# Performance work log

Hardware: AMD Instinct MI355X
Metric: run time of the kernel (lower is better)

The kernel has to match this reference:

```python
import jax, jax.numpy as jnp
import numpy as np

B, T, D = 4096, 64, 100   # trajectories, observed time points, feature dim (50 feat + 50 mask)
F = D // 2                # feature half
L = 64                    # latent_dim
NU = 64                   # n_gru_units / n_ode_units
K = 128                   # number of unique event times (integer grid 0..K-1)
DEC = 1                   # decoder output dim (volume)


def setup_inputs() -> dict:
    key = jax.random.key(0)
    ks = jax.random.split(key, 20)
    data = jax.random.normal(ks[0], (B, T, D), dtype=jnp.float32)
    # make mask half non-negative so (sum>0) masking is meaningful
    data = data.at[:, :, F:].set(jnp.abs(data[:, :, F:]))
    time_steps = jnp.sort(jax.random.randint(ks[1], (B, T), 0, K), axis=1)
    s = 0.1
    p = {}
    gi = D // 2 + L  # GRU gate input: latent + feature half
    p['Wu1'] = jax.random.normal(ks[2], (gi, NU), jnp.float32) * s
    p['bu1'] = jnp.zeros((NU,), jnp.float32)
    p['Wu2'] = jax.random.normal(ks[3], (NU, L), jnp.float32) * s
    p['bu2'] = jnp.zeros((L,), jnp.float32)
    p['Wr1'] = jax.random.normal(ks[4], (gi, NU), jnp.float32) * s
    p['br1'] = jnp.zeros((NU,), jnp.float32)
    p['Wr2'] = jax.random.normal(ks[5], (NU, L), jnp.float32) * s
    p['br2'] = jnp.zeros((L,), jnp.float32)
    p['Wn1'] = jax.random.normal(ks[6], (gi, NU), jnp.float32) * s
    p['bn1'] = jnp.zeros((NU,), jnp.float32)
    p['Wn2'] = jax.random.normal(ks[7], (NU, L), jnp.float32) * s
    p['bn2'] = jnp.zeros((L,), jnp.float32)
    # ODE func (tanh MLP), Euler-integrated one step per event interval
    p['Wo1'] = jax.random.normal(ks[8], (L, NU), jnp.float32) * s
    p['bo1'] = jnp.zeros((NU,), jnp.float32)
    p['Wo2'] = jax.random.normal(ks[9], (NU, L), jnp.float32) * s
    p['bo2'] = jnp.zeros((L,), jnp.float32)
    # decoder latent -> volume
    p['Wd'] = jax.random.normal(ks[10], (L, DEC), jnp.float32) * s
    p['bd'] = jnp.zeros((DEC,), jnp.float32)
    return {'data': data, 'time_steps': time_steps, **p}


def reference(data, time_steps,
              Wu1, bu1, Wu2, bu2,
              Wr1, br1, Wr2, br2,
              Wn1, bn1, Wn2, bn2,
              Wo1, bo1, Wo2, bo2,
              Wd, bd):
    f32 = data.dtype
    # pad one zero row at end of time axis (torch: cat(data, zeros[:,1]))
    data_pad = jnp.concatenate([data, jnp.zeros((B, 1, D), f32)], axis=1)  # [B, T+1, D]

    # presence[b, k] = 1 if event time k observed for trajectory b
    presence = jnp.zeros((B, K), f32).at[jnp.arange(B)[:, None], time_steps].set(1.0)
    upd_all = presence.T  # [K, B]  (update_mask per step)
    # fetched_count before step k = number of observed events with time < k
    counts = jnp.concatenate([jnp.zeros((B, 1), f32), jnp.cumsum(presence, axis=1)[:, :-1]], axis=1)
    idx_all = jnp.clip(counts.astype(jnp.int32), 0, T).T  # [K, B]
    rows = jnp.arange(B)

    def step(prev_y, inp):
        idx_i, upd_i = inp  # [B] int, [B] float
        upd = upd_i[:, None]
        # ODE solver: linspace gives 2 points per unit interval -> one Euler step, dt=1
        y1 = prev_y + jnp.tanh(prev_y @ Wo1 + bo1) @ Wo2 + bo2  # ode_sol end
        vol = prev_y @ Wd + bd  # decoder(ode_sol[:, :-1]) mean over single point = decoder(y0)
        fx = data_pad[rows, idx_i] * upd  # dynamic gather + mask  [B, D]
        feat, msk = fx[:, :F], fx[:, F:]
        yc = jnp.concatenate([y1, feat], axis=-1)
        u = jax.nn.sigmoid(jnp.tanh(yc @ Wu1 + bu1) @ Wu2 + bu2)
        r = jax.nn.sigmoid(jnp.tanh(yc @ Wr1 + br1) @ Wr2 + br2)
        cc = jnp.concatenate([y1 * r, feat], axis=-1)
        ns = jnp.tanh(cc @ Wn1 + bn1) @ Wn2 + bn2
        ny = (1.0 - u) * ns + u * y1
        m = (jnp.sum(msk, axis=-1, keepdims=True) > 0).astype(f32)
        ny = m * ny + (1.0 - m) * y1
        prev_y = ny * upd + y1 * (1.0 - upd)
        return prev_y, vol

    prev_y0 = jnp.zeros((B, L), f32)
    prev_y, volume_dt = jax.lax.scan(step, prev_y0, (idx_all, upd_all))
    volume_dt = jnp.transpose(volume_dt, (1, 0, 2))  # [B, K, DEC]

    # inverse_indices == time_steps values on the integer event grid
    inv = jnp.clip(time_steps[:, :-1], 0, K - 2)
    selected_state = jnp.take_along_axis(volume_dt[:, 1:], inv[:, :, None], axis=1)  # [B, T-1, DEC]
    time_intervals = (time_steps[:, 1:] - time_steps[:, :-1]).astype(f32)
    return prev_y, selected_state, time_intervals
```

## Files before the change

### kernel.cpp

```cpp
#include <hip/hip_runtime.h>


typedef __attribute__((ext_vector_type(8))) _Float16 half8;
typedef __attribute__((ext_vector_type(4))) float floatx4;

#define MFMA(a, b, c) __builtin_amdgcn_mfma_f32_16x16x32_f16((a), (b), (c), 0, 0, 0)

__device__ __forceinline__ float tanhf_fast(float x) {
    float e = __builtin_exp2f(x * 2.8853900817779268f);
    return 1.0f - 2.0f / (e + 1.0f);
}
__device__ __forceinline__ float sigmoidf_fast(float x) {
    float e = __builtin_exp2f(x * -1.4426950408889634f);
    return 1.0f / (1.0f + e);
}

struct W2 { half8 h, l; };

__global__ __launch_bounds__(256, 1)
void lobrm_fused(const float* __restrict__ data,
                 const int*   __restrict__ tsteps,
                 const float* __restrict__ Wu1, const float* __restrict__ bu1,
                 const float* __restrict__ Wu2, const float* __restrict__ bu2,
                 const float* __restrict__ Wr1, const float* __restrict__ br1,
                 const float* __restrict__ Wr2, const float* __restrict__ br2,
                 const float* __restrict__ Wn1, const float* __restrict__ bn1,
                 const float* __restrict__ Wn2, const float* __restrict__ bn2,
                 const float* __restrict__ Wo1, const float* __restrict__ bo1,
                 const float* __restrict__ Wo2, const float* __restrict__ bo2,
                 const float* __restrict__ Wd,  const float* __restrict__ bd,
                 float* __restrict__ out)
{
    __shared__ __align__(16) _Float16 sYh [16 * 72],  sYl [16 * 72];
    __shared__ __align__(16) _Float16 sTh [16 * 72],  sTl [16 * 72];
    __shared__ __align__(16) _Float16 sHuh[16 * 72],  sHul[16 * 72];
    __shared__ __align__(16) _Float16 sHrh[16 * 72],  sHrl[16 * 72];
    __shared__ __align__(16) _Float16 sYCh[16 * 136], sYCl[16 * 136];
    __shared__ __align__(16) _Float16 sCCh[16 * 136], sCCl[16 * 136];
    __shared__ float    sVol[16 * 132];
    __shared__ unsigned sFlg[16];

    const int tid   = threadIdx.x;
    const int lane  = tid & 63;
    const int wv    = tid >> 6;
    const int col16 = lane & 15;
    const int quad  = lane >> 4;
    const int ncol  = wv * 16 + col16;
    const int rowBase = blockIdx.x * 16;

    for (int x = tid; x < 16 * 72; x += 256) {
        sYh[x] = (_Float16)0.f; sYl[x] = (_Float16)0.f;
    }
    for (int x = tid; x < 16 * 136; x += 256) {
        sYCh[x] = (_Float16)0.f; sYCl[x] = (_Float16)0.f;
        sCCh[x] = (_Float16)0.f; sCCl[x] = (_Float16)0.f;
    }
    const float bdv = bd[0];

    auto loadW = [&](const float* W, int Kw, int kb) -> W2 {
        W2 f;
#pragma unroll
        for (int j = 0; j < 8; ++j) {
            int k = kb * 32 + quad * 8 + j;
            float v = (k < Kw) ? W[k * 64 + ncol] : 0.0f;
            _Float16 h = (_Float16)v;
            f.h[j] = h;
            f.l[j] = (_Float16)(v - (float)h);
        }
        return f;
    };
    W2 wO1[2], wO2[2], wU2[2], wR2[2], wN2[2], wU1[4], wR1[4], wN1[4];
#pragma unroll
    for (int kb = 0; kb < 2; ++kb) {
        wO1[kb] = loadW(Wo1, 64, kb);
        wO2[kb] = loadW(Wo2, 64, kb);
        wU2[kb] = loadW(Wu2, 64, kb);
        wR2[kb] = loadW(Wr2, 64, kb);
        wN2[kb] = loadW(Wn2, 64, kb);
    }
#pragma unroll
    for (int kb = 0; kb < 4; ++kb) {
        wU1[kb] = loadW(Wu1, 114, kb);
        wR1[kb] = loadW(Wr1, 114, kb);
        wN1[kb] = loadW(Wn1, 114, kb);
    }
    half8 vwd[2];
#pragma unroll
    for (int kb = 0; kb < 2; ++kb)
#pragma unroll
        for (int j = 0; j < 8; ++j) {
            int k = kb * 32 + quad * 8 + j;
            vwd[kb][j] = (_Float16)((col16 == 0) ? Wd[k] : 0.0f);
        }
    const float bo1v = bo1[ncol], bo2v = bo2[ncol];
    const float bu1v = bu1[ncol], bu2v = bu2[ncol];
    const float br1v = br1[ncol], br2v = br2[ncol];
    const float bn1v = bn1[ncol], bn2v = bn2[ncol];

    unsigned long long mLo[4], mHi[4];
    const float* dPtr[4];
#pragma unroll
    for (int r4 = 0; r4 < 4; ++r4) {
        int b = rowBase + 4 * wv + r4;
        int v = tsteps[b * 64 + lane];
        unsigned long long lo = (v < 64) ? (1ull << v) : 0ull;
        unsigned long long hi = (v >= 64) ? (1ull << (v - 64)) : 0ull;
#pragma unroll
        for (int st = 1; st < 64; st <<= 1) {
            lo |= __shfl_xor(lo, st);
            hi |= __shfl_xor(hi, st);
        }
        mLo[r4] = lo; mHi[r4] = hi;
        dPtr[r4] = data + (size_t)b * 6400;
    }
    __syncthreads();

    floatx4 pc = {0.f, 0.f, 0.f, 0.f};
    const floatx4 z = {0.f, 0.f, 0.f, 0.f};

    const int aOff  = col16 * 72 + quad * 8;
    const int aOffH = col16 * 136 + quad * 8;

    bool hasU[4];
    float fv[4], mv[4];
#pragma unroll
    for (int r4 = 0; r4 < 4; ++r4) {
        hasU[r4] = (mLo[r4] & 1ull) != 0ull;
        fv[r4] = 0.f; mv[r4] = 0.f;
        if (hasU[r4]) {
            const float* dp = dPtr[r4];
            dPtr[r4] = dp + 100;
            if (lane < 50) { fv[r4] = dp[lane]; mv[r4] = dp[50 + lane]; }
        }
    }

    for (int i = 0; i < 128; ++i) {
        const int ip = i + 1;
        bool hasN[4];
        float fN[4], mN[4];
#pragma unroll
        for (int r4 = 0; r4 < 4; ++r4) {
            unsigned long long mm =
                (ip < 64) ? (mLo[r4] >> ip)
                          : ((ip < 128) ? (mHi[r4] >> (ip - 64)) : 0ull);
            hasN[r4] = (mm & 1ull) != 0ull;
            fN[r4] = 0.f; mN[r4] = 0.f;
            if (hasN[r4]) {
                const float* dp = dPtr[r4];
                dPtr[r4] = dp + 100;
                if (lane < 50) { fN[r4] = dp[lane]; mN[r4] = dp[50 + lane]; }
            }
        }

        {
            half8 a0h = *(const half8*)&sYh[aOff];
            half8 a0l = *(const half8*)&sYl[aOff];
            half8 a1h = *(const half8*)&sYh[aOff + 32];
            half8 a1l = *(const half8*)&sYl[aOff + 32];
            floatx4 cb = {bo1v, bo1v, bo1v, bo1v};
            floatx4 hh = MFMA(a1h, wO1[1].h, MFMA(a0h, wO1[0].h, cb));
            floatx4 hl = MFMA(a1h, wO1[1].l, MFMA(a0h, wO1[0].l, z));
            floatx4 lh = MFMA(a1l, wO1[1].h, MFMA(a0l, wO1[0].h, z));
            if (wv == 0) {
                floatx4 v = MFMA(a1h, vwd[1], MFMA(a0h, vwd[0], z));
                if (col16 == 0) {
#pragma unroll
                    for (int r = 0; r < 4; ++r)
                        sVol[(quad * 4 + r) * 132 + i] = v[r] + bdv;
                }
            }
            floatx4 acc = hh + (hl + lh);
#pragma unroll
            for (int r = 0; r < 4; ++r) {
                float t = tanhf_fast(acc[r]);
                _Float16 h = (_Float16)t;
                int idx = (quad * 4 + r) * 72 + ncol;
                sTh[idx] = h;
                sTl[idx] = (_Float16)(t - (float)h);
            }
        }
        __syncthreads();

        floatx4 y1;
        {
            half8 t0h = *(const half8*)&sTh[aOff];
            half8 t0l = *(const half8*)&sTl[aOff];
            half8 t1h = *(const half8*)&sTh[aOff + 32];
            half8 t1l = *(const half8*)&sTl[aOff + 32];
            floatx4 cb = {bo2v, bo2v, bo2v, bo2v};
            floatx4 hh = MFMA(t1h, wO2[1].h, MFMA(t0h, wO2[0].h, cb));
            floatx4 hl = MFMA(t1h, wO2[1].l, MFMA(t0h, wO2[0].l, z));
            floatx4 lh = MFMA(t1l, wO2[1].h, MFMA(t0l, wO2[0].h, z));
            floatx4 acc = hh + (hl + lh);
#pragma unroll
            for (int r = 0; r < 4; ++r) {
                y1[r] = pc[r] + acc[r];
                _Float16 h = (_Float16)y1[r];
                int idx = (quad * 4 + r) * 136 + ncol;
                sYCh[idx] = h;
                sYCl[idx] = (_Float16)(y1[r] - (float)h);
            }
        }

#pragma unroll
        for (int r4 = 0; r4 < 4; ++r4) {
            int row = 4 * wv + r4;
            if (hasU[r4]) {
                if (lane < 50) {
                    float f = fv[r4];
                    _Float16 h = (_Float16)f;
                    _Float16 l = (_Float16)(f - (float)h);
                    int idx = row * 136 + 64 + lane;
                    sYCh[idx] = h; sYCl[idx] = l;
                    sCCh[idx] = h; sCCl[idx] = l;
                }
                unsigned long long bal = __ballot(mv[r4] > 0.f);
                if (lane == 0) sFlg[row] = bal ? 1u : 0u;
            } else if (lane == 0) {
                sFlg[row] = 0u;
            }
        }
        __syncthreads();

        {
            half8 ah0 = *(const half8*)&sYCh[aOffH];
            half8 ah1 = *(const half8*)&sYCh[aOffH + 32];
            half8 ah2 = *(const half8*)&sYCh[aOffH + 64];
            half8 ah3 = *(const half8*)&sYCh[aOffH + 96];
            half8 al0 = *(const half8*)&sYCl[aOffH];
            half8 al1 = *(const half8*)&sYCl[aOffH + 32];
            half8 al2 = *(const half8*)&sYCl[aOffH + 64];
            half8 al3 = *(const half8*)&sYCl[aOffH + 96];
            floatx4 cu = {bu1v, bu1v, bu1v, bu1v};
            floatx4 cr = {br1v, br1v, br1v, br1v};
            floatx4 uhh = MFMA(ah3, wU1[3].h, MFMA(ah2, wU1[2].h,
                          MFMA(ah1, wU1[1].h, MFMA(ah0, wU1[0].h, cu))));
            floatx4 uhl = MFMA(ah3, wU1[3].l, MFMA(ah2, wU1[2].l,
                          MFMA(ah1, wU1[1].l, MFMA(ah0, wU1[0].l, z))));
            floatx4 ulh = MFMA(al3, wU1[3].h, MFMA(al2, wU1[2].h,
                          MFMA(al1, wU1[1].h, MFMA(al0, wU1[0].h, z))));
            floatx4 rhh = MFMA(ah3, wR1[3].h, MFMA(ah2, wR1[2].h,
                          MFMA(ah1, wR1[1].h, MFMA(ah0, wR1[0].h, cr))));
            floatx4 rhl = MFMA(ah3, wR1[3].l, MFMA(ah2, wR1[2].l,
                          MFMA(ah1, wR1[1].l, MFMA(ah0, wR1[0].l, z))));
            floatx4 rlh = MFMA(al3, wR1[3].h, MFMA(al2, wR1[2].h,
                          MFMA(al1, wR1[1].h, MFMA(al0, wR1[0].h, z))));
            floatx4 aU = uhh + (uhl + ulh);
            floatx4 aR = rhh + (rhl + rlh);
#pragma unroll
            for (int r = 0; r < 4; ++r) {
                float tu = tanhf_fast(aU[r]);
                float tr = tanhf_fast(aR[r]);
                int idx = (quad * 4 + r) * 72 + ncol;
                _Float16 hu = (_Float16)tu, hr = (_Float16)tr;
                sHuh[idx] = hu; sHul[idx] = (_Float16)(tu - (float)hu);
                sHrh[idx] = hr; sHrl[idx] = (_Float16)(tr - (float)hr);
            }
        }
        __syncthreads();

        floatx4 uG;
        {
            half8 u0h = *(const half8*)&sHuh[aOff];
            half8 u0l = *(const half8*)&sHul[aOff];
            half8 u1h = *(const half8*)&sHuh[aOff + 32];
            half8 u1l = *(const half8*)&sHul[aOff + 32];
            floatx4 cu = {bu2v, bu2v, bu2v, bu2v};
            floatx4 cr = {br2v, br2v, br2v, br2v};
            floatx4 au = MFMA(u1h, wU2[1].h, MFMA(u0h, wU2[0].h, cu))
                       + (MFMA(u1h, wU2[1].l, MFMA(u0h, wU2[0].l, z))
                        + MFMA(u1l, wU2[1].h, MFMA(u0l, wU2[0].h, z)));
            half8 r0h = *(const half8*)&sHrh[aOff];
            half8 r0l = *(const half8*)&sHrl[aOff];
            half8 r1h = *(const half8*)&sHrh[aOff + 32];
            half8 r1l = *(const half8*)&sHrl[aOff + 32];
            floatx4 ar = MFMA(r1h, wR2[1].h, MFMA(r0h, wR2[0].h, cr))
                       + (MFMA(r1h, wR2[1].l, MFMA(r0h, wR2[0].l, z))
                        + MFMA(r1l, wR2[1].h, MFMA(r0l, wR2[0].h, z)));
#pragma unroll
            for (int r = 0; r < 4; ++r) {
                uG[r] = sigmoidf_fast(au[r]);
                float rg = sigmoidf_fast(ar[r]);
                float cc = y1[r] * rg;
                _Float16 h = (_Float16)cc;
                int idx = (quad * 4 + r) * 136 + ncol;
                sCCh[idx] = h;
                sCCl[idx] = (_Float16)(cc - (float)h);
            }
        }
        __syncthreads();

        {
            half8 ah0 = *(const half8*)&sCCh[aOffH];
            half8 ah1 = *(const half8*)&sCCh[aOffH + 32];
            half8 ah2 = *(const half8*)&sCCh[aOffH + 64];
            half8 ah3 = *(const half8*)&sCCh[aOffH + 96];
            half8 al0 = *(const half8*)&sCCl[aOffH];
            half8 al1 = *(const half8*)&sCCl[aOffH + 32];
            half8 al2 = *(const half8*)&sCCl[aOffH + 64];
            half8 al3 = *(const half8*)&sCCl[aOffH + 96];
            floatx4 cn = {bn1v, bn1v, bn1v, bn1v};
            floatx4 nhh = MFMA(ah3, wN1[3].h, MFMA(ah2, wN1[2].h,
                          MFMA(ah1, wN1[1].h, MFMA(ah0, wN1[0].h, cn))));
            floatx4 nhl = MFMA(ah3, wN1[3].l, MFMA(ah2, wN1[2].l,
                          MFMA(ah1, wN1[1].l, MFMA(ah0, wN1[0].l, z))));
            floatx4 nlh = MFMA(al3, wN1[3].h, MFMA(al2, wN1[2].h,
                          MFMA(al1, wN1[1].h, MFMA(al0, wN1[0].h, z))));
            floatx4 aN = nhh + (nhl + nlh);
#pragma unroll
            for (int r = 0; r < 4; ++r) {
                float t = tanhf_fast(aN[r]);
                _Float16 h = (_Float16)t;
                int idx = (quad * 4 + r) * 72 + ncol;
                sTh[idx] = h;
                sTl[idx] = (_Float16)(t - (float)h);
            }
        }
        __syncthreads();

        {
            half8 n0h = *(const half8*)&sTh[aOff];
            half8 n0l = *(const half8*)&sTl[aOff];
            half8 n1h = *(const half8*)&sTh[aOff + 32];
            half8 n1l = *(const half8*)&sTl[aOff + 32];
            floatx4 cn = {bn2v, bn2v, bn2v, bn2v};
            floatx4 acc = MFMA(n1h, wN2[1].h, MFMA(n0h, wN2[0].h, cn))
                        + (MFMA(n1h, wN2[1].l, MFMA(n0h, wN2[0].l, z))
                         + MFMA(n1l, wN2[1].h, MFMA(n0l, wN2[0].h, z)));
#pragma unroll
            for (int r = 0; r < 4; ++r) {
                float ns = acc[r];
                float ny = (1.0f - uG[r]) * ns + uG[r] * y1[r];
                unsigned ap = sFlg[quad * 4 + r];
                float nY = ap ? ny : y1[r];
                pc[r] = nY;
                int rr = quad * 4 + r;
                _Float16 h = (_Float16)nY;
                sYh[rr * 72 + ncol] = h;
                sYl[rr * 72 + ncol] = (_Float16)(nY - (float)h);
            }
        }
        __syncthreads();

#pragma unroll
        for (int r4 = 0; r4 < 4; ++r4) {
            hasU[r4] = hasN[r4];
            fv[r4] = fN[r4];
            mv[r4] = mN[r4];
        }
    }

#pragma unroll
    for (int r = 0; r < 4; ++r) {
        int b = rowBase + quad * 4 + r;
        out[(size_t)b * 64 + ncol] = pc[r];
    }
    float* out1 = out + (size_t)4096 * 64;
    float* out2 = out1 + (size_t)4096 * 63;
#pragma unroll
    for (int r4 = 0; r4 < 4; ++r4) {
        int row = 4 * wv + r4;
        int b = rowBase + row;
        if (lane < 63) {
            int t0 = tsteps[b * 64 + lane];
            int t1 = tsteps[b * 64 + lane + 1];
            int iv = t0 < 126 ? t0 : 126;
            out1[(size_t)b * 63 + lane] = sVol[row * 132 + iv + 1];
            out2[(size_t)b * 63 + lane] = (float)(t1 - t0);
        }
    }
}

extern "C" void kernel_launch(void* const* d_in, const int* in_sizes, int n_in,
                              void* d_out, int out_size, void* d_ws, size_t ws_size,
                              hipStream_t stream) {
    const float* data   = (const float*)d_in[0];
    const int*   tsteps = (const int*)  d_in[1];
    const float* Wu1 = (const float*)d_in[2];  const float* bu1 = (const float*)d_in[3];
    const float* Wu2 = (const float*)d_in[4];  const float* bu2 = (const float*)d_in[5];
    const float* Wr1 = (const float*)d_in[6];  const float* br1 = (const float*)d_in[7];
    const float* Wr2 = (const float*)d_in[8];  const float* br2 = (const float*)d_in[9];
    const float* Wn1 = (const float*)d_in[10]; const float* bn1 = (const float*)d_in[11];
    const float* Wn2 = (const float*)d_in[12]; const float* bn2 = (const float*)d_in[13];
    const float* Wo1 = (const float*)d_in[14]; const float* bo1 = (const float*)d_in[15];
    const float* Wo2 = (const float*)d_in[16]; const float* bo2 = (const float*)d_in[17];
    const float* Wd  = (const float*)d_in[18]; const float* bd  = (const float*)d_in[19];
    float* out = (float*)d_out;

    lobrm_fused<<<dim3(256), dim3(256), 0, stream>>>(
        data, tsteps, Wu1, bu1, Wu2, bu2, Wr1, br1, Wr2, br2,
        Wn1, bn1, Wn2, bn2, Wo1, bo1, Wo2, bo2, Wd, bd, out);
}
```

Before: 595.7 us.

## Fold ODE output layer into GRU gate weights to cut a barrier per step

A small prep kernel precomputes Wo2·Wu1y and Wo2·Wr1y plus folded biases, so the update and reset gate pre-activations are computed straight from the ODE hidden tanh. This lets y1 be formed in parallel with the gate inputs instead of before them. The feature-side contributions of the gate matmuls are issued early alongside the first ODE layer, and next-step feature staging moves into the last phase with a double-buffered flag array. Together these remove one block-wide barrier and shrink the concatenated LDS buffers per time step. The cost is extra MFMAs, a different floating-point rounding path through the folded weights, more register pressure from added weight fragments, and two tiny extra launches.

```diff
diff --git a/kernel.cpp b/kernel.cpp
--- a/kernel.cpp
+++ b/kernel.cpp
@@ -16,6 +16,31 @@
 }
 
 struct W2 { half8 h, l; };
+
+__global__ __launch_bounds__(256)
+void lobrm_prep(const float* __restrict__ Wo2, const float* __restrict__ WX1,
+                const float* __restrict__ bX1, const float* __restrict__ bo2,
+                float* __restrict__ outW, float* __restrict__ outB)
+{
+    __shared__ float sA[4096], sB[4096];
+    const int tid = threadIdx.x;
+    for (int x = tid; x < 4096; x += 256) { sA[x] = Wo2[x]; sB[x] = WX1[x]; }
+    __syncthreads();
+    const int k = tid >> 2, n0 = (tid & 3) * 16;
+    for (int c = 0; c < 16; ++c) {
+        int n = n0 + c;
+        float acc = 0.f;
+#pragma unroll 8
+        for (int j = 0; j < 64; ++j) acc += sA[k * 64 + j] * sB[j * 64 + n];
+        outW[k * 64 + n] = acc;
+    }
+    if (tid < 64) {
+        float acc = bX1[tid];
+#pragma unroll 8
+        for (int j = 0; j < 64; ++j) acc += bo2[j] * sB[j * 64 + tid];
+        outB[tid] = acc;
+    }
+}
 
 __global__ __launch_bounds__(256, 1)
 void lobrm_fused(const float* __restrict__ data,
@@ -29,16 +54,17 @@
                  const float* __restrict__ Wo1, const float* __restrict__ bo1,
                  const float* __restrict__ Wo2, const float* __restrict__ bo2,
                  const float* __restrict__ Wd,  const float* __restrict__ bd,
+                 const float* __restrict__ ws,
                  float* __restrict__ out)
 {
-    __shared__ __align__(16) _Float16 sYh [16 * 72],  sYl [16 * 72];
-    __shared__ __align__(16) _Float16 sTh [16 * 72],  sTl [16 * 72];
-    __shared__ __align__(16) _Float16 sHuh[16 * 72],  sHul[16 * 72];
-    __shared__ __align__(16) _Float16 sHrh[16 * 72],  sHrl[16 * 72];
-    __shared__ __align__(16) _Float16 sYCh[16 * 136], sYCl[16 * 136];
-    __shared__ __align__(16) _Float16 sCCh[16 * 136], sCCl[16 * 136];
+    __shared__ __align__(16) _Float16 sYh [16 * 72], sYl [16 * 72];
+    __shared__ __align__(16) _Float16 sFh [16 * 72], sFl [16 * 72];
+    __shared__ __align__(16) _Float16 sTh [16 * 72], sTl [16 * 72];
+    __shared__ __align__(16) _Float16 sHuh[16 * 72], sHul[16 * 72];
+    __shared__ __align__(16) _Float16 sHrh[16 * 72], sHrl[16 * 72];
+    __shared__ __align__(16) _Float16 sCCh[16 * 72], sCCl[16 * 72];
     __shared__ float    sVol[16 * 132];
-    __shared__ unsigned sFlg[16];
+    __shared__ unsigned sFlg[2][16];
 
     const int tid   = threadIdx.x;
     const int lane  = tid & 63;
@@ -50,39 +76,39 @@
 
     for (int x = tid; x < 16 * 72; x += 256) {
         sYh[x] = (_Float16)0.f; sYl[x] = (_Float16)0.f;
-    }
-    for (int x = tid; x < 16 * 136; x += 256) {
-        sYCh[x] = (_Float16)0.f; sYCl[x] = (_Float16)0.f;
-        sCCh[x] = (_Float16)0.f; sCCl[x] = (_Float16)0.f;
+        sFh[x] = (_Float16)0.f; sFl[x] = (_Float16)0.f;
     }
     const float bdv = bd[0];
 
-    auto loadW = [&](const float* W, int Kw, int kb) -> W2 {
+    auto loadW = [&](const float* W, int rowOff, int Kw, int kbg) -> W2 {
         W2 f;
 #pragma unroll
         for (int j = 0; j < 8; ++j) {
-            int k = kb * 32 + quad * 8 + j;
-            float v = (k < Kw) ? W[k * 64 + ncol] : 0.0f;
+            int k = kbg * 32 + quad * 8 + j;
+            float v = (k < Kw) ? W[(rowOff + k) * 64 + ncol] : 0.0f;
             _Float16 h = (_Float16)v;
             f.h[j] = h;
             f.l[j] = (_Float16)(v - (float)h);
         }
         return f;
     };
-    W2 wO1[2], wO2[2], wU2[2], wR2[2], wN2[2], wU1[4], wR1[4], wN1[4];
-#pragma unroll
-    for (int kb = 0; kb < 2; ++kb) {
-        wO1[kb] = loadW(Wo1, 64, kb);
-        wO2[kb] = loadW(Wo2, 64, kb);
-        wU2[kb] = loadW(Wu2, 64, kb);
-        wR2[kb] = loadW(Wr2, 64, kb);
-        wN2[kb] = loadW(Wn2, 64, kb);
-    }
-#pragma unroll
-    for (int kb = 0; kb < 4; ++kb) {
-        wU1[kb] = loadW(Wu1, 114, kb);
-        wR1[kb] = loadW(Wr1, 114, kb);
-        wN1[kb] = loadW(Wn1, 114, kb);
+    W2 wO1[2], wO2[2], wO2u[2], wO2r[2], wU2[2], wR2[2], wN2[2];
+    W2 wU1y[2], wU1f[2], wR1y[2], wR1f[2], wN1y[2], wN1f[2];
+#pragma unroll
+    for (int t = 0; t < 2; ++t) {
+        wO1[t]  = loadW(Wo1, 0, 64, t);
+        wO2[t]  = loadW(Wo2, 0, 64, t);
+        wO2u[t] = loadW(ws,        0, 64, t);
+        wO2r[t] = loadW(ws + 4096, 0, 64, t);
+        wU2[t]  = loadW(Wu2, 0, 64, t);
+        wR2[t]  = loadW(Wr2, 0, 64, t);
+        wN2[t]  = loadW(Wn2, 0, 64, t);
+        wU1y[t] = loadW(Wu1, 0, 64, t);
+        wU1f[t] = loadW(Wu1, 64, 50, t);
+        wR1y[t] = loadW(Wr1, 0, 64, t);
+        wR1f[t] = loadW(Wr1, 64, 50, t);
+        wN1y[t] = loadW(Wn1, 0, 64, t);
+        wN1f[t] = loadW(Wn1, 64, 50, t);
     }
     half8 vwd[2];
 #pragma unroll
@@ -93,9 +119,10 @@
             vwd[kb][j] = (_Float16)((col16 == 0) ? Wd[k] : 0.0f);
         }
     const float bo1v = bo1[ncol], bo2v = bo2[ncol];
-    const float bu1v = bu1[ncol], bu2v = bu2[ncol];
-    const float br1v = br1[ncol], br2v = br2[ncol];
+    const float bu2v = bu2[ncol], br2v = br2[ncol];
     const float bn1v = bn1[ncol], bn2v = bn2[ncol];
+    const float bu1pv = ws[8192 + ncol];
+    const float br1pv = ws[8256 + ncol];
 
     unsigned long long mLo[4], mHi[4];
     const float* dPtr[4];
@@ -113,28 +140,88 @@
         mLo[r4] = lo; mHi[r4] = hi;
         dPtr[r4] = data + (size_t)b * 6400;
     }
-    __syncthreads();
-
-    floatx4 pc = {0.f, 0.f, 0.f, 0.f};
-    const floatx4 z = {0.f, 0.f, 0.f, 0.f};
-
-    const int aOff  = col16 * 72 + quad * 8;
-    const int aOffH = col16 * 136 + quad * 8;
-
-    bool hasU[4];
-    float fv[4], mv[4];
+
 #pragma unroll
     for (int r4 = 0; r4 < 4; ++r4) {
-        hasU[r4] = (mLo[r4] & 1ull) != 0ull;
-        fv[r4] = 0.f; mv[r4] = 0.f;
-        if (hasU[r4]) {
+        int row = 4 * wv + r4;
+        bool h0 = (mLo[r4] & 1ull) != 0ull;
+        float f0 = 0.f, m0 = 0.f;
+        if (h0) {
             const float* dp = dPtr[r4];
             dPtr[r4] = dp + 100;
-            if (lane < 50) { fv[r4] = dp[lane]; mv[r4] = dp[50 + lane]; }
-        }
-    }
+            if (lane < 50) { f0 = dp[lane]; m0 = dp[50 + lane]; }
+            if (lane < 50) {
+                _Float16 h = (_Float16)f0;
+                sFh[row * 72 + lane] = h;
+                sFl[row * 72 + lane] = (_Float16)(f0 - (float)h);
+            }
+            unsigned long long bal = __ballot(m0 > 0.f);
+            if (lane == 0) sFlg[0][row] = bal ? 1u : 0u;
+        } else if (lane == 0) {
+            sFlg[0][row] = 0u;
+        }
+    }
+    __syncthreads();
+
+    floatx4 pc = {0.f, 0.f, 0.f, 0.f};
+    const floatx4 z4 = {0.f, 0.f, 0.f, 0.f};
+
+    const int aOff = col16 * 72 + quad * 8;
 
     for (int i = 0; i < 128; ++i) {
+        floatx4 U0, R0, N0, y1, uG;
+        {
+            half8 yh0 = *(const half8*)&sYh[aOff];
+            half8 yh1 = *(const half8*)&sYh[aOff + 32];
+            half8 yl0 = *(const half8*)&sYl[aOff];
+            half8 yl1 = *(const half8*)&sYl[aOff + 32];
+            half8 fh0 = *(const half8*)&sFh[aOff];
+            half8 fh1 = *(const half8*)&sFh[aOff + 32];
+            half8 fl0 = *(const half8*)&sFl[aOff];
+            half8 fl1 = *(const half8*)&sFl[aOff + 32];
+            floatx4 zc = {bo1v, bo1v, bo1v, bo1v};
+            floatx4 zhh = MFMA(yh1, wO1[1].h, MFMA(yh0, wO1[0].h, zc));
+            floatx4 zhl = MFMA(yh1, wO1[1].l, MFMA(yh0, wO1[0].l, z4));
+            floatx4 zlh = MFMA(yl1, wO1[1].h, MFMA(yl0, wO1[0].h, z4));
+            if (wv == 0) {
+                floatx4 v = MFMA(yh1, vwd[1], MFMA(yh0, vwd[0], z4));
+                if (col16 == 0) {
+#pragma unroll
+                    for (int r = 0; r < 4; ++r)
+                        sVol[(quad * 4 + r) * 132 + i] = v[r] + bdv;
+                }
+            }
+            floatx4 cu = {bu1pv, bu1pv, bu1pv, bu1pv};
+            floatx4 uhh = MFMA(fh1, wU1f[1].h, MFMA(fh0, wU1f[0].h,
+                          MFMA(yh1, wU1y[1].h, MFMA(yh0, wU1y[0].h, cu))));
+            floatx4 uhl = MFMA(fh1, wU1f[1].l, MFMA(fh0, wU1f[0].l,
+                          MFMA(yh1, wU1y[1].l, MFMA(yh0, wU1y[0].l, z4))));
+            floatx4 ulh = MFMA(fl1, wU1f[1].h, MFMA(fl0, wU1f[0].h,
+                          MFMA(yl1, wU1y[1].h, MFMA(yl0, wU1y[0].h, z4))));
+            U0 = uhh + (uhl + ulh);
+            floatx4 cr = {br1pv, br1pv, br1pv, br1pv};
+            floatx4 rhh = MFMA(fh1, wR1f[1].h, MFMA(fh0, wR1f[0].h,
+                          MFMA(yh1, wR1y[1].h, MFMA(yh0, wR1y[0].h, cr))));
+            floatx4 rhl = MFMA(fh1, wR1f[1].l, MFMA(fh0, wR1f[0].l,
+                          MFMA(yh1, wR1y[1].l, MFMA(yh0, wR1y[0].l, z4))));
+            floatx4 rlh = MFMA(fl1, wR1f[1].h, MFMA(fl0, wR1f[0].h,
+                          MFMA(yl1, wR1y[1].h, MFMA(yl0, wR1y[0].h, z4))));
+            R0 = rhh + (rhl + rlh);
+            floatx4 cn = {bn1v, bn1v, bn1v, bn1v};
+            floatx4 nhh = MFMA(fh1, wN1f[1].h, MFMA(fh0, wN1f[0].h, cn));
+            floatx4 nhl = MFMA(fh1, wN1f[1].l, MFMA(fh0, wN1f[0].l, z4));
+            floatx4 nlh = MFMA(fl1, wN1f[1].h, MFMA(fl0, wN1f[0].h, z4));
+            N0 = nhh + (nhl + nlh);
+            floatx4 zacc = zhh + (zhl + zlh);
+#pragma unroll
+            for (int r = 0; r < 4; ++r) {
+                float t = tanhf_fast(zacc[r]);
+                _Float16 h = (_Float16)t;
+                int idx = (quad * 4 + r) * 72 + ncol;
+                sTh[idx] = h;
+                sTl[idx] = (_Float16)(t - (float)h);
+            }
+        }
         const int ip = i + 1;
         bool hasN[4];
         float fN[4], mN[4];
@@ -151,106 +238,31 @@
                 if (lane < 50) { fN[r4] = dp[lane]; mN[r4] = dp[50 + lane]; }
             }
         }
+        __syncthreads();
 
         {
-            half8 a0h = *(const half8*)&sYh[aOff];
-            half8 a0l = *(const half8*)&sYl[aOff];
-            half8 a1h = *(const half8*)&sYh[aOff + 32];
-            half8 a1l = *(const half8*)&sYl[aOff + 32];
-            floatx4 cb = {bo1v, bo1v, bo1v, bo1v};
-            floatx4 hh = MFMA(a1h, wO1[1].h, MFMA(a0h, wO1[0].h, cb));
-            floatx4 hl = MFMA(a1h, wO1[1].l, MFMA(a0h, wO1[0].l, z));
-            floatx4 lh = MFMA(a1l, wO1[1].h, MFMA(a0l, wO1[0].h, z));
-            if (wv == 0) {
-                floatx4 v = MFMA(a1h, vwd[1], MFMA(a0h, vwd[0], z));
-                if (col16 == 0) {
-#pragma unroll
-                    for (int r = 0; r < 4; ++r)
-                        sVol[(quad * 4 + r) * 132 + i] = v[r] + bdv;
-                }
-            }
-            floatx4 acc = hh + (hl + lh);
+            half8 th0 = *(const half8*)&sTh[aOff];
+            half8 th1 = *(const half8*)&sTh[aOff + 32];
+            half8 tl0 = *(const half8*)&sTl[aOff];
+            half8 tl1 = *(const half8*)&sTl[aOff + 32];
+            floatx4 cb = {bo2v, bo2v, bo2v, bo2v};
+            floatx4 yhh = MFMA(th1, wO2[1].h, MFMA(th0, wO2[0].h, cb));
+            floatx4 yhl = MFMA(th1, wO2[1].l, MFMA(th0, wO2[0].l, z4));
+            floatx4 ylh = MFMA(tl1, wO2[1].h, MFMA(tl0, wO2[0].h, z4));
+            floatx4 yacc = yhh + (yhl + ylh);
+            floatx4 uhh = MFMA(th1, wO2u[1].h, MFMA(th0, wO2u[0].h, U0));
+            floatx4 uhl = MFMA(th1, wO2u[1].l, MFMA(th0, wO2u[0].l, z4));
+            floatx4 ulh = MFMA(tl1, wO2u[1].h, MFMA(tl0, wO2u[0].h, z4));
+            floatx4 hua = uhh + (uhl + ulh);
+            floatx4 rhh = MFMA(th1, wO2r[1].h, MFMA(th0, wO2r[0].h, R0));
+            floatx4 rhl = MFMA(th1, wO2r[1].l, MFMA(th0, wO2r[0].l, z4));
+            floatx4 rlh = MFMA(tl1, wO2r[1].h, MFMA(tl0, wO2r[0].h, z4));
+            floatx4 hra = rhh + (rhl + rlh);
 #pragma unroll
             for (int r = 0; r < 4; ++r) {
-                float t = tanhf_fast(acc[r]);
-                _Float16 h = (_Float16)t;
-                int idx = (quad * 4 + r) * 72 + ncol;
-                sTh[idx] = h;
-                sTl[idx] = (_Float16)(t - (float)h);
-            }
-        }
-        __syncthreads();
-
-        floatx4 y1;
-        {
-            half8 t0h = *(const half8*)&sTh[aOff];
-            half8 t0l = *(const half8*)&sTl[aOff];
-            half8 t1h = *(const half8*)&sTh[aOff + 32];
-            half8 t1l = *(const half8*)&sTl[aOff + 32];
-            floatx4 cb = {bo2v, bo2v, bo2v, bo2v};
-            floatx4 hh = MFMA(t1h, wO2[1].h, MFMA(t0h, wO2[0].h, cb));
-            floatx4 hl = MFMA(t1h, wO2[1].l, MFMA(t0h, wO2[0].l, z));
-            floatx4 lh = MFMA(t1l, wO2[1].h, MFMA(t0l, wO2[0].h, z));
-            floatx4 acc = hh + (hl + lh);
-#pragma unroll
-            for (int r = 0; r < 4; ++r) {
-                y1[r] = pc[r] + acc[r];
-                _Float16 h = (_Float16)y1[r];
-                int idx = (quad * 4 + r) * 136 + ncol;
-                sYCh[idx] = h;
-                sYCl[idx] = (_Float16)(y1[r] - (float)h);
-            }
-        }
-
-#pragma unroll
-        for (int r4 = 0; r4 < 4; ++r4) {
-            int row = 4 * wv + r4;
-            if (hasU[r4]) {
-                if (lane < 50) {
-                    float f = fv[r4];
-                    _Float16 h = (_Float16)f;
-                    _Float16 l = (_Float16)(f - (float)h);
-                    int idx = row * 136 + 64 + lane;
-                    sYCh[idx] = h; sYCl[idx] = l;
-                    sCCh[idx] = h; sCCl[idx] = l;
-                }
-                unsigned long long bal = __ballot(mv[r4] > 0.f);
-                if (lane == 0) sFlg[row] = bal ? 1u : 0u;
-            } else if (lane == 0) {
-                sFlg[row] = 0u;
-            }
-        }
-        __syncthreads();
-
-        {
-            half8 ah0 = *(const half8*)&sYCh[aOffH];
-            half8 ah1 = *(const half8*)&sYCh[aOffH + 32];
-            half8 ah2 = *(const half8*)&sYCh[aOffH + 64];
-            half8 ah3 = *(const half8*)&sYCh[aOffH + 96];
-            half8 al0 = *(const half8*)&sYCl[aOffH];
-            half8 al1 = *(const half8*)&sYCl[aOffH + 32];
-            half8 al2 = *(const half8*)&sYCl[aOffH + 64];
-            half8 al3 = *(const half8*)&sYCl[aOffH + 96];
-            floatx4 cu = {bu1v, bu1v, bu1v, bu1v};
-            floatx4 cr = {br1v, br1v, br1v, br1v};
-            floatx4 uhh = MFMA(ah3, wU1[3].h, MFMA(ah2, wU1[2].h,
-                          MFMA(ah1, wU1[1].h, MFMA(ah0, wU1[0].h, cu))));
-            floatx4 uhl = MFMA(ah3, wU1[3].l, MFMA(ah2, wU1[2].l,
-                          MFMA(ah1, wU1[1].l, MFMA(ah0, wU1[0].l, z))));
-            floatx4 ulh = MFMA(al3, wU1[3].h, MFMA(al2, wU1[2].h,
-                          MFMA(al1, wU1[1].h, MFMA(al0, wU1[0].h, z))));
-            floatx4 rhh = MFMA(ah3, wR1[3].h, MFMA(ah2, wR1[2].h,
-                          MFMA(ah1, wR1[1].h, MFMA(ah0, wR1[0].h, cr))));
-            floatx4 rhl = MFMA(ah3, wR1[3].l, MFMA(ah2, wR1[2].l,
-                          MFMA(ah1, wR1[1].l, MFMA(ah0, wR1[0].l, z))));
-            floatx4 rlh = MFMA(al3, wR1[3].h, MFMA(al2, wR1[2].h,
-                          MFMA(al1, wR1[1].h, MFMA(al0, wR1[0].h, z))));
-            floatx4 aU = uhh + (uhl + ulh);
-            floatx4 aR = rhh + (rhl + rlh);
-#pragma unroll
-            for (int r = 0; r < 4; ++r) {
-                float tu = tanhf_fast(aU[r]);
-                float tr = tanhf_fast(aR[r]);
+                y1[r] = pc[r] + yacc[r];
+                float tu = tanhf_fast(hua[r]);
+                float tr = tanhf_fast(hra[r]);
                 int idx = (quad * 4 + r) * 72 + ncol;
                 _Float16 hu = (_Float16)tu, hr = (_Float16)tr;
                 sHuh[idx] = hu; sHul[idx] = (_Float16)(tu - (float)hu);
@@ -259,31 +271,30 @@
         }
         __syncthreads();
 
-        floatx4 uG;
         {
             half8 u0h = *(const half8*)&sHuh[aOff];
             half8 u0l = *(const half8*)&sHul[aOff];
             half8 u1h = *(const half8*)&sHuh[aOff + 32];
             half8 u1l = *(const half8*)&sHul[aOff + 32];
             floatx4 cu = {bu2v, bu2v, bu2v, bu2v};
-            floatx4 cr = {br2v, br2v, br2v, br2v};
             floatx4 au = MFMA(u1h, wU2[1].h, MFMA(u0h, wU2[0].h, cu))
-                       + (MFMA(u1h, wU2[1].l, MFMA(u0h, wU2[0].l, z))
-                        + MFMA(u1l, wU2[1].h, MFMA(u0l, wU2[0].h, z)));
+                       + (MFMA(u1h, wU2[1].l, MFMA(u0h, wU2[0].l, z4))
+                        + MFMA(u1l, wU2[1].h, MFMA(u0l, wU2[0].h, z4)));
             half8 r0h = *(const half8*)&sHrh[aOff];
             half8 r0l = *(const half8*)&sHrl[aOff];
             half8 r1h = *(const half8*)&sHrh[aOff + 32];
             half8 r1l = *(const half8*)&sHrl[aOff + 32];
+            floatx4 cr = {br2v, br2v, br2v, br2v};
             floatx4 ar = MFMA(r1h, wR2[1].h, MFMA(r0h, wR2[0].h, cr))
-                       + (MFMA(r1h, wR2[1].l, MFMA(r0h, wR2[0].l, z))
-                        + MFMA(r1l, wR2[1].h, MFMA(r0l, wR2[0].h, z)));
+                       + (MFMA(r1h, wR2[1].l, MFMA(r0h, wR2[0].l, z4))
+                        + MFMA(r1l, wR2[1].h, MFMA(r0l, wR2[0].h, z4)));
 #pragma unroll
             for (int r = 0; r < 4; ++r) {
                 uG[r] = sigmoidf_fast(au[r]);
                 float rg = sigmoidf_fast(ar[r]);
                 float cc = y1[r] * rg;
                 _Float16 h = (_Float16)cc;
-                int idx = (quad * 4 + r) * 136 + ncol;
+                int idx = (quad * 4 + r) * 72 + ncol;
                 sCCh[idx] = h;
                 sCCl[idx] = (_Float16)(cc - (float)h);
             }
@@ -291,25 +302,17 @@
         __syncthreads();
 
         {
-            half8 ah0 = *(const half8*)&sCCh[aOffH];
-            half8 ah1 = *(const half8*)&sCCh[aOffH + 32];
-            half8 ah2 = *(const half8*)&sCCh[aOffH + 64];
-            half8 ah3 = *(const half8*)&sCCh[aOffH + 96];
-            half8 al0 = *(const half8*)&sCCl[aOffH];
-            half8 al1 = *(const half8*)&sCCl[aOffH + 32];
-            half8 al2 = *(const half8*)&sCCl[aOffH + 64];
-            half8 al3 = *(const half8*)&sCCl[aOffH + 96];
-            floatx4 cn = {bn1v, bn1v, bn1v, bn1v};
-            floatx4 nhh = MFMA(ah3, wN1[3].h, MFMA(ah2, wN1[2].h,
-                          MFMA(ah1, wN1[1].h, MFMA(ah0, wN1[0].h, cn))));
-            floatx4 nhl = MFMA(ah3, wN1[3].l, MFMA(ah2, wN1[2].l,
-                          MFMA(ah1, wN1[1].l, MFMA(ah0, wN1[0].l, z))));
-            floatx4 nlh = MFMA(al3, wN1[3].h, MFMA(al2, wN1[2].h,
-                          MFMA(al1, wN1[1].h, MFMA(al0, wN1[0].h, z))));
-            floatx4 aN = nhh + (nhl + nlh);
+            half8 ch0 = *(const half8*)&sCCh[aOff];
+            half8 ch1 = *(const half8*)&sCCh[aOff + 32];
+            half8 cl0 = *(const half8*)&sCCl[aOff];
+            half8 cl1 = *(const half8*)&sCCl[aOff + 32];
+            floatx4 nhh = MFMA(ch1, wN1y[1].h, MFMA(ch0, wN1y[0].h, N0));
+            floatx4 nhl = MFMA(ch1, wN1y[1].l, MFMA(ch0, wN1y[0].l, z4));
+            floatx4 nlh = MFMA(cl1, wN1y[1].h, MFMA(cl0, wN1y[0].h, z4));
+            floatx4 hna = nhh + (nhl + nlh);
 #pragma unroll
             for (int r = 0; r < 4; ++r) {
-                float t = tanhf_fast(aN[r]);
+                float t = tanhf_fast(hna[r]);
                 _Float16 h = (_Float16)t;
                 int idx = (quad * 4 + r) * 72 + ncol;
                 sTh[idx] = h;
@@ -325,29 +328,38 @@
             half8 n1l = *(const half8*)&sTl[aOff + 32];
             floatx4 cn = {bn2v, bn2v, bn2v, bn2v};
             floatx4 acc = MFMA(n1h, wN2[1].h, MFMA(n0h, wN2[0].h, cn))
-                        + (MFMA(n1h, wN2[1].l, MFMA(n0h, wN2[0].l, z))
-                         + MFMA(n1l, wN2[1].h, MFMA(n0l, wN2[0].h, z)));
+                        + (MFMA(n1h, wN2[1].l, MFMA(n0h, wN2[0].l, z4))
+                         + MFMA(n1l, wN2[1].h, MFMA(n0l, wN2[0].h, z4)));
 #pragma unroll
             for (int r = 0; r < 4; ++r) {
                 float ns = acc[r];
                 float ny = (1.0f - uG[r]) * ns + uG[r] * y1[r];
-                unsigned ap = sFlg[quad * 4 + r];
+                unsigned ap = sFlg[i & 1][quad * 4 + r];
                 float nY = ap ? ny : y1[r];
                 pc[r] = nY;
-                int rr = quad * 4 + r;
+                int idx = (quad * 4 + r) * 72 + ncol;
                 _Float16 h = (_Float16)nY;
-                sYh[rr * 72 + ncol] = h;
-                sYl[rr * 72 + ncol] = (_Float16)(nY - (float)h);
+                sYh[idx] = h;
+                sYl[idx] = (_Float16)(nY - (float)h);
+            }
+#pragma unroll
+            for (int r4 = 0; r4 < 4; ++r4) {
+                int row = 4 * wv + r4;
+                if (hasN[r4]) {
+                    if (lane < 50) {
+                        float f = fN[r4];
+                        _Float16 h = (_Float16)f;
+                        sFh[row * 72 + lane] = h;
+                        sFl[row * 72 + lane] = (_Float16)(f - (float)h);
+                    }
+                    unsigned long long bal = __ballot(mN[r4] > 0.f);
+                    if (lane == 0) sFlg[(i + 1) & 1][row] = bal ? 1u : 0u;
+                } else if (lane == 0) {
+                    sFlg[(i + 1) & 1][row] = 0u;
+                }
             }
         }
         __syncthreads();
-
-#pragma unroll
-        for (int r4 = 0; r4 < 4; ++r4) {
-            hasU[r4] = hasN[r4];
-            fv[r4] = fN[r4];
-            mv[r4] = mN[r4];
-        }
     }
 
 #pragma unroll
@@ -386,8 +398,12 @@
     const float* Wo2 = (const float*)d_in[16]; const float* bo2 = (const float*)d_in[17];
     const float* Wd  = (const float*)d_in[18]; const float* bd  = (const float*)d_in[19];
     float* out = (float*)d_out;
+    float* ws  = (float*)d_ws;
+
+    lobrm_prep<<<dim3(1), dim3(256), 0, stream>>>(Wo2, Wu1, bu1, bo2, ws, ws + 8192);
+    lobrm_prep<<<dim3(1), dim3(256), 0, stream>>>(Wo2, Wr1, br1, bo2, ws + 4096, ws + 8192 + 64);
 
     lobrm_fused<<<dim3(256), dim3(256), 0, stream>>>(
         data, tsteps, Wu1, bu1, Wu2, bu2, Wr1, br1, Wr2, br2,
-        Wn1, bn1, Wn2, bn2, Wo1, bo1, Wo2, bo2, Wd, bd, out);
+        Wn1, bn1, Wn2, bn2, Wo1, bo1, Wo2, bo2, Wd, bd, ws, out);
 }
```

Measured after the change: 687.4 us. 1.15x slower.
